# Kernel tuning notes

Hardware: AMD Instinct MI355X
Metric: run time of the kernel (lower is better)

The kernel has to match this reference:

```python
import jax, jax.numpy as jnp
import numpy as np

DEPTH = 10
NUM_FEATURES = 512
NUM_LEAVES = 2 ** DEPTH
TEMPERATURE = 0.1
BATCH = 32768


def _leaf_codes():
    # codes[leaf, i] = bit i (MSB first) of leaf index
    leaves = np.arange(NUM_LEAVES)
    shifts = DEPTH - 1 - np.arange(DEPTH)
    codes = (leaves[:, None] >> shifts[None, :]) & 1
    return jnp.asarray(codes, dtype=jnp.float32)  # [num_leaves, depth]


def setup_inputs() -> dict:
    key = jax.random.key(0)
    k1, k2, k3 = jax.random.split(key, 3)
    x = jax.random.normal(k1, (BATCH, NUM_FEATURES), dtype=jnp.float32)
    feature_weights = jax.random.normal(k2, (DEPTH, NUM_FEATURES), dtype=jnp.float32) * 0.01
    thresholds = jnp.zeros((DEPTH,), dtype=jnp.float32)
    leaf_values = jax.random.normal(k3, (NUM_FEATURES, NUM_LEAVES), dtype=jnp.float32) * 0.01
    return {"x": x, "feature_weights": feature_weights,
            "thresholds": thresholds, "leaf_values": leaf_values}


def reference(x, feature_weights, thresholds, leaf_values):
    codes = _leaf_codes()                                   # [L, D]
    probs = jax.nn.softmax(feature_weights, axis=1)          # [D, F]
    sel = x @ probs.T                                        # [B, D]
    decisions = jax.nn.sigmoid((sel - thresholds) / TEMPERATURE)  # [B, D]
    # leaf_probs[b, l] = prod_d (p*code + (1-p)*(1-code))
    p = decisions[:, None, :]                                # [B, 1, D]
    c = codes[None, :, :]                                    # [1, L, D]
    leaf_probs = jnp.prod(p * c + (1.0 - p) * (1.0 - c), axis=-1)  # [B, L]
    out = leaf_probs @ leaf_values.T                         # [B, F]
    return out
```

## Files before the change

### kernel.cpp

```cpp
#include <hip/hip_runtime.h>
#include <hip/hip_bf16.h>
#include <cstdint>

using u16 = unsigned short;
using u32 = unsigned int;

#define DEPTH 10
#define NF 512
#define NL 1024
#define BATCH_N 32768
#define TEMP_INV 10.0f
#define GBM 128
#define GBN 256
#define GBK 32
#define NSTEP 32

typedef float f32x4 __attribute__((ext_vector_type(4)));
typedef short s16x8 __attribute__((ext_vector_type(8)));
typedef __bf16 bf16x8 __attribute__((ext_vector_type(8)));

__device__ __forceinline__ u16 f2bf(float f) {
  u32 u = __float_as_uint(f);
  u = (u + 0x7fffu + ((u >> 16) & 1u)) >> 16;
  return (u16)u;
}

__device__ __forceinline__ void gld_lds16(const void* g, void* lds) {
  __builtin_amdgcn_global_load_lds(
      (const __attribute__((address_space(1))) void*)g,
      (__attribute__((address_space(3))) void*)lds, 16, 0, 0);
}

__global__ void k_cvt(const float* __restrict__ lv, u16* __restrict__ lvb) {
  int i = (blockIdx.x * blockDim.x + threadIdx.x) * 8;
  float4 a = *(const float4*)(lv + i);
  float4 b = *(const float4*)(lv + i + 4);
  uint4 u;
  u.x = f2bf(a.x) | ((u32)f2bf(a.y) << 16);
  u.y = f2bf(a.z) | ((u32)f2bf(a.w) << 16);
  u.z = f2bf(b.x) | ((u32)f2bf(b.y) << 16);
  u.w = f2bf(b.z) | ((u32)f2bf(b.w) << 16);
  *(uint4*)(lvb + i) = u;
}

__global__ __launch_bounds__(256, 4) void k_sel(const float* __restrict__ x,
                                                const float* __restrict__ fw,
                                                const float* __restrict__ thr,
                                                float* __restrict__ pout) {
  __shared__ float Ps[DEPTH * NF];
  const int tid = threadIdx.x;
  const int lane = tid & 63;
  const int w = tid >> 6;

  for (int d = w; d < DEPTH; d += 4) {
    const float* row = fw + d * NF;
    float v[8];
    float mx = -1e30f;
#pragma unroll
    for (int i = 0; i < 8; ++i) { v[i] = row[lane * 8 + i]; mx = fmaxf(mx, v[i]); }
#pragma unroll
    for (int s = 32; s >= 1; s >>= 1) mx = fmaxf(mx, __shfl_xor(mx, s));
    float sum = 0.f;
#pragma unroll
    for (int i = 0; i < 8; ++i) { v[i] = __expf(v[i] - mx); sum += v[i]; }
#pragma unroll
    for (int s = 32; s >= 1; s >>= 1) sum += __shfl_xor(sum, s);
    float inv = 1.0f / sum;
#pragma unroll
    for (int i = 0; i < 8; ++i) Ps[d * NF + lane * 8 + i] = v[i] * inv;
  }
  __syncthreads();

  const int g = lane & 15;
  const int qr = lane >> 4;
  const int r0 = blockIdx.x * 32 + (w * 4 + qr) * 2;
  const float* xp0 = x + (size_t)r0 * NF + g * 4;
  const float* xp1 = xp0 + NF;

  float a0[DEPTH], a1[DEPTH];
#pragma unroll
  for (int d = 0; d < DEPTH; ++d) { a0[d] = 0.f; a1[d] = 0.f; }
#pragma unroll 2
  for (int i = 0; i < 8; ++i) {
    float4 xv0 = *(const float4*)(xp0 + i * 64);
    float4 xv1 = *(const float4*)(xp1 + i * 64);
    const float* pb = &Ps[i * 64 + g * 4];
#pragma unroll
    for (int d = 0; d < DEPTH; ++d) {
      f32x4 pv = *(const f32x4*)(pb + d * NF);
      a0[d] += xv0.x * pv[0] + xv0.y * pv[1] + xv0.z * pv[2] + xv0.w * pv[3];
      a1[d] += xv1.x * pv[0] + xv1.y * pv[1] + xv1.z * pv[2] + xv1.w * pv[3];
    }
  }
#pragma unroll
  for (int d = 0; d < DEPTH; ++d) {
    a0[d] += __shfl_xor(a0[d], 1); a0[d] += __shfl_xor(a0[d], 2);
    a0[d] += __shfl_xor(a0[d], 4); a0[d] += __shfl_xor(a0[d], 8);
    a1[d] += __shfl_xor(a1[d], 1); a1[d] += __shfl_xor(a1[d], 2);
    a1[d] += __shfl_xor(a1[d], 4); a1[d] += __shfl_xor(a1[d], 8);
  }
  if (g < DEPTH) {
    float s0 = (g == 0) ? a0[0] : (g == 1) ? a0[1] : (g == 2) ? a0[2]
             : (g == 3) ? a0[3] : (g == 4) ? a0[4] : (g == 5) ? a0[5]
             : (g == 6) ? a0[6] : (g == 7) ? a0[7] : (g == 8) ? a0[8] : a0[9];
    float s1 = (g == 0) ? a1[0] : (g == 1) ? a1[1] : (g == 2) ? a1[2]
             : (g == 3) ? a1[3] : (g == 4) ? a1[4] : (g == 5) ? a1[5]
             : (g == 6) ? a1[6] : (g == 7) ? a1[7] : (g == 8) ? a1[8] : a1[9];
    float t = thr[g];
    pout[(size_t)r0 * DEPTH + g]       = 1.0f / (1.0f + __expf(-(s0 - t) * TEMP_INV));
    pout[(size_t)(r0 + 1) * DEPTH + g] = 1.0f / (1.0f + __expf(-(s1 - t) * TEMP_INV));
  }
}

__global__ __launch_bounds__(256, 2) void k_gemm(const u16* __restrict__ B,
                                                 const float* __restrict__ p,
                                                 float* __restrict__ C) {
  __shared__ char smem[65536];
  const int tid = threadIdx.x;
  const int lane = tid & 63;
  const int w = tid >> 6;
  const int wm = w >> 1, wn = w & 1;
  const int bm = blockIdx.x >> 1, bn = blockIdx.x & 1;
  const int brow = bm * GBM, bcol = bn * GBN;

  const int gr = tid >> 1;
  const int gh = tid & 1;
  const float* prw = p + (size_t)(brow + gr) * DEPTH;
  float pv[10];
#pragma unroll
  for (int d = 0; d < 10; ++d) pv[d] = prw[d];
  float T[16];
  {
    float s5 = gh ? pv[5] : 1.f - pv[5];
    float a6 = 1.f - pv[6], b6 = pv[6], a7 = 1.f - pv[7], b7 = pv[7];
    float a8 = 1.f - pv[8], b8 = pv[8], a9 = 1.f - pv[9], b9 = pv[9];
    float m67[4] = {a6 * a7, a6 * b7, b6 * a7, b6 * b7};
    float m89[4] = {a8 * a9, a8 * b9, b8 * a9, b8 * b9};
#pragma unroll
    for (int i = 0; i < 16; ++i) T[i] = s5 * m67[i >> 2] * m89[i & 3];
  }
  const float p0a = 1.f - pv[0], p0b = pv[0], p1a = 1.f - pv[1], p1b = pv[1],
              p2a = 1.f - pv[2], p2b = pv[2], p3a = 1.f - pv[3], p3b = pv[3],
              p4a = 1.f - pv[4], p4b = pv[4];

  const int xorg = (gr >> 1) & 3;
  const int wb0 = gr * 64 + (((gh * 2)     ^ xorg) << 4);
  const int wb1 = gr * 64 + (((gh * 2 + 1) ^ xorg) << 4);

  f32x4 acc[4][8];
#pragma unroll
  for (int m = 0; m < 4; ++m)
#pragma unroll
    for (int n = 0; n < 8; ++n) acc[m][n] = {0.f, 0.f, 0.f, 0.f};

  auto STAGE = [&](int step, int buf) {
    char* bsb = smem + buf * 16384;
#pragma unroll
    for (int it = 0; it < 4; ++it) {
      int lin = it * 256 + tid;
      int r = lin >> 2;
      int slog = (lin & 3) ^ ((r >> 1) & 3);
      gld_lds16(B + (size_t)(bcol + r) * NL + step * GBK + slog * 8, bsb + lin * 16);
    }
  };
  auto GENA = [&](int step, int buf) {
    float H = ((step & 16) ? p0b : p0a) * ((step & 8) ? p1b : p1a);
    H *= (step & 4) ? p2b : p2a;
    H *= (step & 2) ? p3b : p3a;
    H *= (step & 1) ? p4b : p4a;
    bf16x8 v0, v1;
#pragma unroll
    for (int j = 0; j < 8; ++j) {
      v0[j] = (__bf16)(H * T[j]);
      v1[j] = (__bf16)(H * T[8 + j]);
    }
    char* asb = smem + 49152 + buf * 8192;
    *(bf16x8*)(asb + wb0) = v0;
    *(bf16x8*)(asb + wb1) = v1;
  };

  const int rA = lane & 15, sg = lane >> 4;
  const int soff = (sg ^ ((rA >> 1) & 3)) << 4;
  const int aoff = (wm * 64 + rA) * 64 + soff;
  const int boff = (wn * 128 + rA) * 64 + soff;

  auto DOMFMA = [&](int bbuf, int abuf) {
    const char* ab = smem + 49152 + abuf * 8192;
    const char* bb = smem + bbuf * 16384;
    bf16x8 a[4];
#pragma unroll
    for (int m = 0; m < 4; ++m)
      a[m] = __builtin_bit_cast(bf16x8, *(const s16x8*)(ab + aoff + m * 1024));
#pragma unroll
    for (int n = 0; n < 8; ++n) {
      bf16x8 bf = __builtin_bit_cast(bf16x8, *(const s16x8*)(bb + boff + n * 1024));
      acc[0][n] = __builtin_amdgcn_mfma_f32_16x16x32_bf16(a[0], bf, acc[0][n], 0, 0, 0);
      acc[1][n] = __builtin_amdgcn_mfma_f32_16x16x32_bf16(a[1], bf, acc[1][n], 0, 0, 0);
      acc[2][n] = __builtin_amdgcn_mfma_f32_16x16x32_bf16(a[2], bf, acc[2][n], 0, 0, 0);
      acc[3][n] = __builtin_amdgcn_mfma_f32_16x16x32_bf16(a[3], bf, acc[3][n], 0, 0, 0);
    }
  };

  STAGE(0, 0);
  GENA(0, 0);
  STAGE(1, 1);

  int bcur = 0, bpre = 2;
  for (int kk = 0; kk < NSTEP - 1; ++kk) {
    asm volatile("s_waitcnt vmcnt(4) lgkmcnt(0)" ::: "memory");
    __builtin_amdgcn_s_barrier();
    __builtin_amdgcn_sched_barrier(0);
    if (kk < NSTEP - 2) STAGE(kk + 2, bpre);
    GENA(kk + 1, (kk + 1) & 1);
    DOMFMA(bcur, kk & 1);
    bcur = (bcur == 2) ? 0 : bcur + 1;
    bpre = (bpre == 2) ? 0 : bpre + 1;
  }
  asm volatile("s_waitcnt vmcnt(0) lgkmcnt(0)" ::: "memory");
  __builtin_amdgcn_s_barrier();
  __builtin_amdgcn_sched_barrier(0);
  DOMFMA(bcur, (NSTEP - 1) & 1);

  const int c0 = lane & 15;
  const int r0 = (lane >> 4) * 4;
#pragma unroll
  for (int m = 0; m < 4; ++m)
#pragma unroll
    for (int n = 0; n < 8; ++n) {
      int col = bcol + wn * 128 + n * 16 + c0;
#pragma unroll
      for (int r = 0; r < 4; ++r)
        C[(size_t)(brow + wm * 64 + m * 16 + r0 + r) * NF + col] = acc[m][n][r];
    }
}

extern "C" void kernel_launch(void* const* d_in, const int* in_sizes, int n_in,
                              void* d_out, int out_size, void* d_ws, size_t ws_size,
                              hipStream_t stream) {
  const float* x  = (const float*)d_in[0];
  const float* fw = (const float*)d_in[1];
  const float* th = (const float*)d_in[2];
  const float* lv = (const float*)d_in[3];
  float* out = (float*)d_out;

  u16* lvb = (u16*)d_ws;
  float* pbuf = (float*)((char*)d_ws + NF * NL * 2);

  k_cvt<<<(NF * NL / 8) / 256, 256, 0, stream>>>(lv, lvb);
  k_sel<<<BATCH_N / 32, 256, 0, stream>>>(x, fw, th, pbuf);
  k_gemm<<<(BATCH_N / GBM) * 2, 256, 0, stream>>>(lvb, pbuf, out);
}
```

Before: 64.30 us.

## Generate A fragments in registers and double-buffer 64-wide B tiles

The leaf-probability A tile is no longer written to and read from LDS. Each lane now builds its MFMA A fragments directly in registers, using precomputed per-row ratios and a base product. The K tile grows to 64 with a new XOR swizzle, and the triple-buffered B pipeline becomes a double buffer with one barrier per step. This removes the LDS traffic and barriers tied to A, at the cost of more VALU and conversion work per lane, more registers, and a full vmcnt(0) wait each step that limits load/compute overlap. Computing leaf probabilities as p/(1-p) ratios also risks inf or NaN when a decision probability is exactly 1.

Result: slower. 67.23 us (+4.6%).

```diff
diff --git a/kernel.cpp b/kernel.cpp
--- a/kernel.cpp
+++ b/kernel.cpp
@@ -12,8 +12,8 @@
 #define TEMP_INV 10.0f
 #define GBM 128
 #define GBN 256
-#define GBK 32
-#define NSTEP 32
+#define GBK 64
+#define NSTEP (NL / GBK)
 
 typedef float f32x4 __attribute__((ext_vector_type(4)));
 typedef short s16x8 __attribute__((ext_vector_type(8)));
@@ -122,30 +122,25 @@
   const int wm = w >> 1, wn = w & 1;
   const int bm = blockIdx.x >> 1, bn = blockIdx.x & 1;
   const int brow = bm * GBM, bcol = bn * GBN;
-
-  const int gr = tid >> 1;
-  const int gh = tid & 1;
-  const float* prw = p + (size_t)(brow + gr) * DEPTH;
-  float pv[10];
-#pragma unroll
-  for (int d = 0; d < 10; ++d) pv[d] = prw[d];
-  float T[16];
-  {
-    float s5 = gh ? pv[5] : 1.f - pv[5];
-    float a6 = 1.f - pv[6], b6 = pv[6], a7 = 1.f - pv[7], b7 = pv[7];
-    float a8 = 1.f - pv[8], b8 = pv[8], a9 = 1.f - pv[9], b9 = pv[9];
-    float m67[4] = {a6 * a7, a6 * b7, b6 * a7, b6 * b7};
-    float m89[4] = {a8 * a9, a8 * b9, b8 * a9, b8 * b9};
-#pragma unroll
-    for (int i = 0; i < 16; ++i) T[i] = s5 * m67[i >> 2] * m89[i & 3];
-  }
-  const float p0a = 1.f - pv[0], p0b = pv[0], p1a = 1.f - pv[1], p1b = pv[1],
-              p2a = 1.f - pv[2], p2b = pv[2], p3a = 1.f - pv[3], p3b = pv[3],
-              p4a = 1.f - pv[4], p4b = pv[4];
-
-  const int xorg = (gr >> 1) & 3;
-  const int wb0 = gr * 64 + (((gh * 2)     ^ xorg) << 4);
-  const int wb1 = gr * 64 + (((gh * 2 + 1) ^ xorg) << 4);
+  const int rA = lane & 15, sg = lane >> 4;
+
+  float T[4][8];
+  float base0[4], r0_[4], r1_[4], r2_[4], r3_[4], r4_[4];
+#pragma unroll
+  for (int m = 0; m < 4; ++m) {
+    const float* pr = p + (size_t)(brow + wm * 64 + m * 16 + rA) * DEPTH;
+    float p0 = pr[0], p1 = pr[1], p2 = pr[2], p3 = pr[3], p4 = pr[4];
+    float p5 = pr[5], p6 = pr[6], p7 = pr[7], p8 = pr[8], p9 = pr[9];
+    float q0 = 1.f - p0, q1 = 1.f - p1, q2 = 1.f - p2, q3 = 1.f - p3, q4 = 1.f - p4;
+    base0[m] = q0 * q1 * q2 * q3 * q4;
+    r0_[m] = p0 / q0; r1_[m] = p1 / q1; r2_[m] = p2 / q2;
+    r3_[m] = p3 / q3; r4_[m] = p4 / q4;
+    float s56 = ((sg & 2) ? p5 : 1.f - p5) * ((sg & 1) ? p6 : 1.f - p6);
+    float a7 = 1.f - p7, b7 = p7, a8 = 1.f - p8, b8 = p8, a9 = 1.f - p9, b9 = p9;
+#pragma unroll
+    for (int j = 0; j < 8; ++j)
+      T[m][j] = s56 * ((j & 4) ? b7 : a7) * ((j & 2) ? b8 : a8) * ((j & 1) ? b9 : a9);
+  }
 
   f32x4 acc[4][8];
 #pragma unroll
@@ -154,75 +149,78 @@
     for (int n = 0; n < 8; ++n) acc[m][n] = {0.f, 0.f, 0.f, 0.f};
 
   auto STAGE = [&](int step, int buf) {
-    char* bsb = smem + buf * 16384;
-#pragma unroll
-    for (int it = 0; it < 4; ++it) {
+    char* bsb = smem + buf * 32768;
+#pragma unroll
+    for (int it = 0; it < 8; ++it) {
       int lin = it * 256 + tid;
-      int r = lin >> 2;
-      int slog = (lin & 3) ^ ((r >> 1) & 3);
-      gld_lds16(B + (size_t)(bcol + r) * NL + step * GBK + slog * 8, bsb + lin * 16);
+      int r = lin >> 3;
+      int sl = (lin & 7) ^ (r & 7);
+      gld_lds16(B + (size_t)(bcol + r) * NL + step * GBK + sl * 8, bsb + lin * 16);
     }
   };
-  auto GENA = [&](int step, int buf) {
-    float H = ((step & 16) ? p0b : p0a) * ((step & 8) ? p1b : p1a);
-    H *= (step & 4) ? p2b : p2a;
-    H *= (step & 2) ? p3b : p3a;
-    H *= (step & 1) ? p4b : p4a;
-    bf16x8 v0, v1;
-#pragma unroll
-    for (int j = 0; j < 8; ++j) {
-      v0[j] = (__bf16)(H * T[j]);
-      v1[j] = (__bf16)(H * T[8 + j]);
-    }
-    char* asb = smem + 49152 + buf * 8192;
-    *(bf16x8*)(asb + wb0) = v0;
-    *(bf16x8*)(asb + wb1) = v1;
-  };
-
-  const int rA = lane & 15, sg = lane >> 4;
-  const int soff = (sg ^ ((rA >> 1) & 3)) << 4;
-  const int aoff = (wm * 64 + rA) * 64 + soff;
-  const int boff = (wn * 128 + rA) * 64 + soff;
-
-  auto DOMFMA = [&](int bbuf, int abuf) {
-    const char* ab = smem + 49152 + abuf * 8192;
-    const char* bb = smem + bbuf * 16384;
-    bf16x8 a[4];
-#pragma unroll
-    for (int m = 0; m < 4; ++m)
-      a[m] = __builtin_bit_cast(bf16x8, *(const s16x8*)(ab + aoff + m * 1024));
-#pragma unroll
-    for (int n = 0; n < 8; ++n) {
-      bf16x8 bf = __builtin_bit_cast(bf16x8, *(const s16x8*)(bb + boff + n * 1024));
-      acc[0][n] = __builtin_amdgcn_mfma_f32_16x16x32_bf16(a[0], bf, acc[0][n], 0, 0, 0);
-      acc[1][n] = __builtin_amdgcn_mfma_f32_16x16x32_bf16(a[1], bf, acc[1][n], 0, 0, 0);
-      acc[2][n] = __builtin_amdgcn_mfma_f32_16x16x32_bf16(a[2], bf, acc[2][n], 0, 0, 0);
-      acc[3][n] = __builtin_amdgcn_mfma_f32_16x16x32_bf16(a[3], bf, acc[3][n], 0, 0, 0);
-    }
-  };
 
   STAGE(0, 0);
-  GENA(0, 0);
-  STAGE(1, 1);
-
-  int bcur = 0, bpre = 2;
-  for (int kk = 0; kk < NSTEP - 1; ++kk) {
-    asm volatile("s_waitcnt vmcnt(4) lgkmcnt(0)" ::: "memory");
-    __builtin_amdgcn_s_barrier();
-    __builtin_amdgcn_sched_barrier(0);
-    if (kk < NSTEP - 2) STAGE(kk + 2, bpre);
-    GENA(kk + 1, (kk + 1) & 1);
-    DOMFMA(bcur, kk & 1);
-    bcur = (bcur == 2) ? 0 : bcur + 1;
-    bpre = (bpre == 2) ? 0 : bpre + 1;
-  }
-  asm volatile("s_waitcnt vmcnt(0) lgkmcnt(0)" ::: "memory");
+  asm volatile("s_waitcnt vmcnt(0)" ::: "memory");
   __builtin_amdgcn_s_barrier();
-  __builtin_amdgcn_sched_barrier(0);
-  DOMFMA(bcur, (NSTEP - 1) & 1);
+
+#pragma unroll 1
+  for (int kk = 0; kk < NSTEP; ++kk) {
+    if (kk < NSTEP - 1) STAGE(kk + 1, (kk + 1) & 1);
+    const char* bb = smem + (kk & 1) * 32768;
+
+    float H[4];
+#pragma unroll
+    for (int m = 0; m < 4; ++m) {
+      float g = base0[m] * ((kk & 8) ? r0_[m] : 1.0f);
+      g *= (kk & 4) ? r1_[m] : 1.0f;
+      g *= (kk & 2) ? r2_[m] : 1.0f;
+      g *= (kk & 1) ? r3_[m] : 1.0f;
+      H[m] = g;
+    }
+    {
+      bf16x8 af[4];
+#pragma unroll
+      for (int m = 0; m < 4; ++m)
+#pragma unroll
+        for (int j = 0; j < 8; ++j) af[m][j] = (__bf16)(H[m] * T[m][j]);
+#pragma unroll
+      for (int n = 0; n < 8; ++n) {
+        int row = wn * 128 + n * 16 + rA;
+        bf16x8 bf = __builtin_bit_cast(bf16x8,
+            *(const s16x8*)(bb + row * 128 + ((sg ^ (row & 7)) << 4)));
+        acc[0][n] = __builtin_amdgcn_mfma_f32_16x16x32_bf16(af[0], bf, acc[0][n], 0, 0, 0);
+        acc[1][n] = __builtin_amdgcn_mfma_f32_16x16x32_bf16(af[1], bf, acc[1][n], 0, 0, 0);
+        acc[2][n] = __builtin_amdgcn_mfma_f32_16x16x32_bf16(af[2], bf, acc[2][n], 0, 0, 0);
+        acc[3][n] = __builtin_amdgcn_mfma_f32_16x16x32_bf16(af[3], bf, acc[3][n], 0, 0, 0);
+      }
+    }
+    {
+      bf16x8 af[4];
+#pragma unroll
+      for (int m = 0; m < 4; ++m) {
+        float h1 = H[m] * r4_[m];
+#pragma unroll
+        for (int j = 0; j < 8; ++j) af[m][j] = (__bf16)(h1 * T[m][j]);
+      }
+#pragma unroll
+      for (int n = 0; n < 8; ++n) {
+        int row = wn * 128 + n * 16 + rA;
+        bf16x8 bf = __builtin_bit_cast(bf16x8,
+            *(const s16x8*)(bb + row * 128 + (((4 + sg) ^ (row & 7)) << 4)));
+        acc[0][n] = __builtin_amdgcn_mfma_f32_16x16x32_bf16(af[0], bf, acc[0][n], 0, 0, 0);
+        acc[1][n] = __builtin_amdgcn_mfma_f32_16x16x32_bf16(af[1], bf, acc[1][n], 0, 0, 0);
+        acc[2][n] = __builtin_amdgcn_mfma_f32_16x16x32_bf16(af[2], bf, acc[2][n], 0, 0, 0);
+        acc[3][n] = __builtin_amdgcn_mfma_f32_16x16x32_bf16(af[3], bf, acc[3][n], 0, 0, 0);
+      }
+    }
+    if (kk < NSTEP - 1) {
+      asm volatile("s_waitcnt vmcnt(0) lgkmcnt(0)" ::: "memory");
+      __builtin_amdgcn_s_barrier();
+    }
+  }
 
   const int c0 = lane & 15;
-  const int r0 = (lane >> 4) * 4;
+  const int rr = (lane >> 4) * 4;
 #pragma unroll
   for (int m = 0; m < 4; ++m)
 #pragma unroll
@@ -230,7 +228,7 @@
       int col = bcol + wn * 128 + n * 16 + c0;
 #pragma unroll
       for (int r = 0; r < 4; ++r)
-        C[(size_t)(brow + wm * 64 + m * 16 + r0 + r) * NF + col] = acc[m][n][r];
+        C[(size_t)(brow + wm * 64 + m * 16 + rr + r) * NF + col] = acc[m][n][r];
     }
 }
 
```
